# Kernel tuning notes

Hardware: AMD Instinct MI355X
Metric: run time of the kernel (lower is better)

Reference implementation:

```python
import jax, jax.numpy as jnp
import numpy as np

B, L, E = 64, 512, 512       # batch, encoder length, encoder dim
T = 512                      # decoder steps
S, P = 512, 256              # symbols_embedding_dim, prenet_dim
A, D = 1024, 1024            # attention_rnn_dim, decoder_rnn_dim
G, V = 128, 148              # gmm hidden, n_symbols


def setup_inputs() -> dict:
    key = jax.random.key(0)
    ks = jax.random.split(key, 20)
    w = lambda k, shp, s=0.02: (jax.random.normal(k, shp, dtype=jnp.float32) * s)
    memory = jax.random.normal(ks[0], (B, L, E), dtype=jnp.float32)
    decoder_inputs = jax.random.normal(ks[1], (B, S, T), dtype=jnp.float32)
    memory_lengths = jax.random.randint(ks[2], (B,), L // 2, L + 1)
    memory_lengths = memory_lengths.at[0].set(L)  # max length == L (static shapes)
    return {
        'memory': memory,
        'decoder_inputs': decoder_inputs,
        'memory_lengths': memory_lengths,
        'W_pre1': w(ks[3], (S, P)), 'W_pre2': w(ks[4], (P, P)),
        'W_att_ih': w(ks[5], (P + E, 4 * A)), 'W_att_hh': w(ks[6], (A, 4 * A)),
        'b_att_ih': jnp.zeros((4 * A,), jnp.float32), 'b_att_hh': jnp.zeros((4 * A,), jnp.float32),
        'W_g1': w(ks[7], (A, G)), 'b_g1': jnp.zeros((G,), jnp.float32),
        'W_g2': w(ks[8], (G, 2), 0.01),  # original inits this to zero; small random to exercise math
        'W_dec_ih': w(ks[9], (A + E, 4 * D)), 'W_dec_hh': w(ks[10], (D, 4 * D)),
        'b_dec_ih': jnp.zeros((4 * D,), jnp.float32), 'b_dec_hh': jnp.zeros((4 * D,), jnp.float32),
        'W_proj': w(ks[11], (D + E, V)), 'b_proj': jnp.zeros((V,), jnp.float32),
    }


def _lstm_cell(x, h, c, Wih, Whh, bih, bhh):
    # torch.nn.LSTMCell gate order: i, f, g, o
    g = x @ Wih + h @ Whh + bih + bhh
    i, f, gg, o = jnp.split(g, 4, axis=-1)
    c = jax.nn.sigmoid(f) * c + jax.nn.sigmoid(i) * jnp.tanh(gg)
    h = jax.nn.sigmoid(o) * jnp.tanh(c)
    return h, c


def _forward(memory, decoder_inputs, memory_lengths,
             W_pre1, W_pre2, W_att_ih, W_att_hh, b_att_ih, b_att_hh,
             W_g1, b_g1, W_g2, W_dec_ih, W_dec_hh, b_dec_ih, b_dec_hh,
             W_proj, b_proj):
    Bv, Sv, Tv = decoder_inputs.shape
    Lv = memory.shape[1]
    # go frame + teacher-forced inputs: (T+1, B, S)
    x = jnp.concatenate([jnp.zeros((1, Bv, Sv), memory.dtype),
                         jnp.transpose(decoder_inputs, (2, 0, 1))], axis=0)
    # Prenet: dropout is hardcoded training=True in the original
    dk1, dk2 = jax.random.split(jax.random.key(42))
    h1 = jax.nn.relu(x @ W_pre1)
    h1 = h1 * jax.random.bernoulli(dk1, 0.5, h1.shape).astype(h1.dtype) * 2.0
    h2 = jax.nn.relu(h1 @ W_pre2)
    pre = h2 * jax.random.bernoulli(dk2, 0.5, h2.shape).astype(h2.dtype) * 2.0  # (T+1,B,P)

    pad_mask = jnp.arange(Lv)[None, :] >= memory_lengths[:, None]  # (B,L) True on padding
    lin = jnp.arange(Lv, dtype=memory.dtype)[None, :]              # (1,L)

    Av, Dv, Ev = W_att_hh.shape[0], W_dec_hh.shape[0], memory.shape[2]
    init = (jnp.zeros((Bv, Av), memory.dtype), jnp.zeros((Bv, Av), memory.dtype),
            jnp.zeros((Bv, Dv), memory.dtype), jnp.zeros((Bv, Dv), memory.dtype),
            jnp.zeros((Bv, Lv), memory.dtype),  # cumulative attention weights
            jnp.zeros((Bv, Ev), memory.dtype),  # attention context
            jnp.zeros((Bv, 1), memory.dtype))   # GMM mean mu

    def step(carry, x_t):
        ah, ac, dh, dc, cum, ctx, mean = carry
        ah, ac = _lstm_cell(jnp.concatenate([x_t, ctx], -1), ah, ac,
                            W_att_ih, W_att_hh, b_att_ih, b_att_hh)
        # (eval mode: p_attention_dropout inactive)
        h = jnp.tanh(ah @ W_g1 + b_g1) @ W_g2          # (B,2) raw [mean_delta, scale]
        mean = mean + jnp.exp(h[:, :1]) * 8.0
        scale = jnp.exp(h[:, 1:]) * 8.0
        Z = jnp.sqrt(2.0 * np.pi * scale * scale)
        alpha = jnp.exp(-0.5 * (lin - mean) ** 2 / (scale * scale)) / Z  # (B,L)
        alpha = jnp.where(pad_mask, 0.0, alpha)
        ctx = jnp.einsum('bl,ble->be', alpha, memory)
        cum = cum + alpha
        dh, dc = _lstm_cell(jnp.concatenate([ah, ctx], -1), dh, dc,
                            W_dec_ih, W_dec_hh, b_dec_ih, b_dec_hh)
        logit = jnp.concatenate([dh, ctx], -1) @ W_proj + b_proj
        return (ah, ac, dh, dc, cum, ctx, mean), (logit, alpha, h)

    _, (logits, aligns, params) = jax.lax.scan(step, init, pre[:-1])
    return (jnp.transpose(logits, (1, 0, 2)),   # (B,T,V)
            jnp.transpose(aligns, (1, 0, 2)),   # (B,T,L)
            jnp.transpose(params, (1, 0, 2)))   # (B,T,2)


def reference(memory, decoder_inputs, memory_lengths, W_pre1, W_pre2,
              W_att_ih, W_att_hh, b_att_ih, b_att_hh, W_g1, b_g1, W_g2,
              W_dec_ih, W_dec_hh, b_dec_ih, b_dec_hh, W_proj, b_proj):
    return _forward(memory, decoder_inputs, memory_lengths, W_pre1, W_pre2,
                    W_att_ih, W_att_hh, b_att_ih, b_att_hh, W_g1, b_g1, W_g2,
                    W_dec_ih, W_dec_hh, b_dec_ih, b_dec_hh, W_proj, b_proj)
```

## Files before the change

### kernel.cpp

```cpp
#include <hip/hip_runtime.h>
#include <math.h>

#define TF_PARTITIONABLE 1

static constexpr int Bn=64, Ln=512, En=512, Tn=512, Sn=512, Pn=256, An=1024, Dn=1024, Gn=128, Vn=148;
static constexpr int G4A = 4096;
static constexpr int KPROJ = Dn + En;
static constexpr int KATT = 1792, KDEC = 2560;
static constexpr int ACH = 4, ACK = 448;
static constexpr int DCH = 4, DCK = 640;
static constexpr int NKB_ATT = KATT / 32;
static constexpr int NKB_DEC = KDEC / 32;
static constexpr long LOGITS_OFF = 0;
static constexpr long ALIGNS_OFF = (long)Bn*Tn*Vn;
static constexpr long PARAMS_OFF = ALIGNS_OFF + (long)Bn*Tn*Ln;

using s16x8 = __attribute__((ext_vector_type(8))) short;
using f32x4 = __attribute__((ext_vector_type(4))) float;

struct TFo { unsigned a, b; };
static constexpr TFo htf(unsigned k1, unsigned k2, unsigned x0, unsigned x1) {
  unsigned ks2 = k1 ^ k2 ^ 0x1BD11BDAu;
  unsigned ks[3] = {k1, k2, ks2};
  const unsigned ra[4] = {13u,15u,26u,6u}, rb[4] = {17u,29u,16u,24u};
  x0 += k1; x1 += k2;
  for (int g = 0; g < 5; ++g) {
    const unsigned* r = (g % 2 == 0) ? ra : rb;
    for (int i = 0; i < 4; ++i) { x0 += x1; x1 = (x1 << r[i]) | (x1 >> (32u - r[i])); x1 ^= x0; }
    x0 += ks[(g+1)%3]; x1 += ks[(g+2)%3] + (unsigned)(g+1);
  }
  return TFo{x0, x1};
}
#if TF_PARTITIONABLE
static constexpr TFo DK1 = htf(0u,42u,0u,0u);
static constexpr TFo DK2 = htf(0u,42u,0u,1u);
#else
static constexpr TFo S02 = htf(0u,42u,0u,2u);
static constexpr TFo S13 = htf(0u,42u,1u,3u);
static constexpr TFo DK1 = TFo{S02.a, S13.a};
static constexpr TFo DK2 = TFo{S02.b, S13.b};
#endif

__device__ __forceinline__ void dtf(unsigned k1, unsigned k2, unsigned x0, unsigned x1,
                                    unsigned& o0, unsigned& o1) {
  unsigned ks2 = k1 ^ k2 ^ 0x1BD11BDAu;
#define TFR(r) { x0 += x1; x1 = (x1<<r)|(x1>>(32-r)); x1 ^= x0; }
  x0 += k1; x1 += k2;
  TFR(13) TFR(15) TFR(26) TFR(6)  x0 += k2;  x1 += ks2 + 1u;
  TFR(17) TFR(29) TFR(16) TFR(24) x0 += ks2; x1 += k1 + 2u;
  TFR(13) TFR(15) TFR(26) TFR(6)  x0 += k1;  x1 += k2 + 3u;
  TFR(17) TFR(29) TFR(16) TFR(24) x0 += k2;  x1 += ks2 + 4u;
  TFR(13) TFR(15) TFR(26) TFR(6)  x0 += ks2; x1 += k1 + 5u;
#undef TFR
  o0 = x0; o1 = x1;
}

__device__ __forceinline__ bool keepmask(unsigned ka, unsigned kb, unsigned j) {
#if TF_PARTITIONABLE
  unsigned o0, o1; dtf(ka, kb, 0u, j, o0, o1);
  return ((o0 ^ o1) >> 31) == 0u;
#else
  const unsigned H = 4202496u;
  unsigned o0, o1;
  if (j < H) { dtf(ka, kb, j, j + H, o0, o1); return (o0 >> 31) == 0u; }
  else       { dtf(ka, kb, j - H, j, o0, o1); return (o1 >> 31) == 0u; }
#endif
}

__device__ __forceinline__ float ldbf(const unsigned short* p, long i) {
  return __uint_as_float(((unsigned)p[i]) << 16);
}
__device__ __forceinline__ unsigned short f2bf(float v) {
  unsigned x = __float_as_uint(v);
  return (unsigned short)((x + 0x7fffu + ((x >> 16) & 1u)) >> 16);
}
__device__ __forceinline__ void store_out(void* out, long i, float v, int bf) {
  if (bf) ((unsigned short*)out)[i] = f2bf(v);
  else    ((float*)out)[i] = v;
}
__device__ __forceinline__ float st_load(const float* p, long i) { return p[i]; }
__device__ __forceinline__ float st_load(const unsigned short* p, long i) { return ldbf(p, i); }
__device__ __forceinline__ void st_store(float* p, long i, float v) { p[i] = v; }
__device__ __forceinline__ void st_store(unsigned short* p, long i, float v) { p[i] = f2bf(v); }
__device__ __forceinline__ float sigm(float x) { return 1.f / (1.f + expf(-x)); }
__device__ __forceinline__ void st4bf(unsigned short* p, float a, float b, float c, float d) {
  union { unsigned short u[4]; uint2 v; } q;
  q.u[0] = f2bf(a); q.u[1] = f2bf(b); q.u[2] = f2bf(c); q.u[3] = f2bf(d);
  *(uint2*)p = q.v;
}
__device__ __forceinline__ void st8bf(unsigned short* p, const float* h) {
  union { unsigned short u[8]; uint4 v; } q;
#pragma unroll
  for (int i = 0; i < 8; ++i) q.u[i] = f2bf(h[i]);
  *(uint4*)p = q.v;
}

struct Ptrs {
  const float *Wp1,*Wp2,*bai,*bah,*Wg1,*bg1,*Wg2,*bdi,*bdh,*Wpr,*bpr;
  unsigned short *PWatt,*PWdec,*pre_bf,*attA,*decA;
  float *Patt,*Pdec,*ac,*dc,*mean;
  void *dh_all,*ctx_all;
  const void *mem,*din,*w_ai,*w_ah,*w_di,*w_dh;
  const int *mlen; const int *flag; void *out;
};

__global__ __launch_bounds__(256) void k_detect(const void* mem, int* flag) {
  __shared__ int cnt;
  int tid = threadIdx.x;
  if (tid == 0) cnt = 0;
  __syncthreads();
  const unsigned short* p = (const unsigned short*)mem;
  int local = 0;
  for (int i = tid; i < 1024; i += 256) {
    float f = ldbf(p, 2L * i);
    if (f == f && fabsf(f) > 0.0009f && fabsf(f) < 16.f) local++;
  }
  atomicAdd(&cnt, local);
  __syncthreads();
  if (tid == 0) flag[0] = (cnt > 512) ? 1 : 0;
}

__global__ __launch_bounds__(256) void k_convert(const void* src, float* dst, long n, const int* flag) {
  int bf = *flag;
  long i0 = (long)blockIdx.x * 256 + threadIdx.x, stp = (long)gridDim.x * 256;
  if (bf) { const unsigned short* s = (const unsigned short*)src;
            for (long i = i0; i < n; i += stp) dst[i] = ldbf(s, i); }
  else    { const float* s = (const float*)src;
            for (long i = i0; i < n; i += stp) dst[i] = s[i]; }
}

__global__ __launch_bounds__(256) void k_zero_f32(float* p, long n) {
  for (long i = (long)blockIdx.x * 256 + threadIdx.x; i < n; i += (long)gridDim.x * 256) p[i] = 0.f;
}

__global__ __launch_bounds__(256) void k_zero_aligns(void* out, const int* flag) {
  int bf = *flag;
  unsigned* p; long n;
  if (bf) { p = (unsigned*)out + (ALIGNS_OFF >> 1); n = ((long)Bn*Tn*Ln) >> 1; }
  else    { p = (unsigned*)out + ALIGNS_OFF;        n = (long)Bn*Tn*Ln; }
  for (long i = (long)blockIdx.x * 256 + threadIdx.x; i < n; i += (long)gridDim.x * 256) p[i] = 0u;
}

__global__ __launch_bounds__(256) void k_precopy(Ptrs P) {
  int tid = threadIdx.x;
  for (int i = tid; i < 2048; i += 256) {
    int b = i >> 5, g = i & 31;
    *(uint4*)(P.attA + (long)b * KATT + g * 8) =
        *(const uint4*)(P.pre_bf + (long)b * Pn + g * 8);
  }
}

__global__ __launch_bounds__(256) void k_pack(Ptrs P) {
  __shared__ float s[32][65];
  int bid = blockIdx.x, tid = threadIdx.x;
  bool att = bid < NKB_ATT * 64;
  int lb = att ? bid : bid - NKB_ATT * 64;
  int kblk = lb >> 6, ng = lb & 63;
  int n0 = ng * 64;
  int bf = *P.flag;
  int split = att ? (Pn + En) : (An + En);
  const void* S0 = att ? P.w_ai : P.w_di;
  const void* S1 = att ? P.w_ah : P.w_dh;
  for (int i = tid; i < 2048; i += 256) {
    int kk = i >> 6, n = i & 63;
    int k = kblk * 32 + kk;
    const void* src = (k < split) ? S0 : S1;
    long idx = (long)(k < split ? k : k - split) * G4A + (n0 + n);
    s[kk][n] = bf ? ldbf((const unsigned short*)src, idx) : ((const float*)src)[idx];
  }
  __syncthreads();
  int lane = tid & 63, tb = tid >> 6;
  unsigned short r[8];
#pragma unroll
  for (int j = 0; j < 8; ++j)
    r[j] = f2bf(s[(lane >> 4) * 8 + j][tb * 16 + (lane & 15)]);
  unsigned short* out = (att ? P.PWatt : P.PWdec) +
      (((long)kblk * 256 + (ng * 4 + tb)) * 64 + lane) * 8;
  *(uint4*)out = *(const uint4*)r;
}

__global__ __launch_bounds__(256) void k_prenet(Ptrs P, unsigned k1a, unsigned k1b,
                                                unsigned k2a, unsigned k2b) {
  __shared__ __align__(16) float x_s[32 * 17];
  __shared__ __align__(16) float W_s[16 * 256];
  __shared__ __align__(16) float h1_s[32 * 258];
  int bid = blockIdx.x, tid = threadIdx.x;
  int t = bid >> 1, half = bid & 1;
  int bf = *P.flag;
  int tc = tid & 63, tr = tid >> 6;
  int p0 = tc * 4, bl0 = tr * 8;
  float acc[8][4];
#pragma unroll
  for (int i = 0; i < 8; ++i) { acc[i][0]=0; acc[i][1]=0; acc[i][2]=0; acc[i][3]=0; }

  for (int kc = 0; kc < 32; ++kc) {
    __syncthreads();
    for (int i = tid; i < 32 * 16; i += 256) {
      int bl = i >> 4, kk = i & 15;
      int s = kc * 16 + kk;
      float v = 0.f;
      if (t > 0) {
        long idx = ((long)(half * 32 + bl) * Sn + s) * Tn + (t - 1);
        v = bf ? ldbf((const unsigned short*)P.din, idx) : ((const float*)P.din)[idx];
      }
      x_s[bl * 17 + kk] = v;
    }
    for (int i = tid; i < 16 * 256; i += 256) {
      int kk = i >> 8, p = i & 255;
      W_s[kk * 256 + p] = P.Wp1[(long)(kc * 16 + kk) * 256 + p];
    }
    __syncthreads();
    for (int kk = 0; kk < 16; ++kk) {
      float4 w = *(const float4*)(W_s + kk * 256 + p0);
#pragma unroll
      for (int i = 0; i < 8; ++i) {
        float x = x_s[(bl0 + i) * 17 + kk];
        acc[i][0] += x * w.x; acc[i][1] += x * w.y; acc[i][2] += x * w.z; acc[i][3] += x * w.w;
      }
    }
  }
#pragma unroll
  for (int i = 0; i < 8; ++i)
#pragma unroll
    for (int j = 0; j < 4; ++j) {
      int bl = bl0 + i, p = p0 + j, bg = half * 32 + bl;
      float v = fmaxf(acc[i][j], 0.f);
      unsigned ft = (unsigned)(((long)t * 64 + bg) * 256 + p);
      v = keepmask(k1a, k1b, ft) ? 2.f * v : 0.f;
      h1_s[bl * 258 + p] = v;
      acc[i][j] = 0.f;
    }
  __syncthreads();
  for (int kc = 0; kc < 16; ++kc) {
    __syncthreads();
    for (int i = tid; i < 16 * 256; i += 256) {
      int kk = i >> 8, p = i & 255;
      W_s[kk * 256 + p] = P.Wp2[(long)(kc * 16 + kk) * 256 + p];
    }
    __syncthreads();
    for (int kk = 0; kk < 16; ++kk) {
      float4 w = *(const float4*)(W_s + kk * 256 + p0);
      int s = kc * 16 + kk;
#pragma unroll
      for (int i = 0; i < 8; ++i) {
        float x = h1_s[(bl0 + i) * 258 + s];
        acc[i][0] += x * w.x; acc[i][1] += x * w.y; acc[i][2] += x * w.z; acc[i][3] += x * w.w;
      }
    }
  }
#pragma unroll
  for (int i = 0; i < 8; ++i)
#pragma unroll
    for (int j = 0; j < 4; ++j) {
      int bg = half * 32 + bl0 + i, p = p0 + j;
      float v = fmaxf(acc[i][j], 0.f);
      unsigned ft = (unsigned)(((long)t * 64 + bg) * 256 + p);
      v = keepmask(k2a, k2b, ft) ? 2.f * v : 0.f;
      P.pre_bf[((long)t * 64 + bg) * 256 + p] = f2bf(v);
    }
}

template<bool ATT>
__device__ __forceinline__ void dev_gemm(const Ptrs& P, int cg, int kc, unsigned short* a_lds) {
  constexpr int CK    = ATT ? ACK : DCK;
  constexpr int SUBK  = CK / 2;
  constexpr int NKS   = SUBK / 32;
  constexpr int PITCH = SUBK + 8;
  constexpr int GPR   = SUBK / 8;
  constexpr int KSTR  = ATT ? KATT : KDEC;
  int tid = threadIdx.x;
  int lane = tid & 63, w = tid >> 6;
  int nblk = cg * 4 + w;
  const unsigned short* PW = ATT ? P.PWatt : P.PWdec;
  const unsigned short* A  = ATT ? P.attA : P.decA;
  int rlo = lane & 15, khi8 = (lane >> 4) * 8;
  const int k0 = kc * CK;

  f32x4 acc[4];
#pragma unroll
  for (int i = 0; i < 4; ++i) acc[i] = f32x4{0.f, 0.f, 0.f, 0.f};

#pragma unroll
  for (int sub = 0; sub < 2; ++sub) {
    const int kk0 = k0 + sub * SUBK;
    __syncthreads();
#pragma unroll
    for (int i = 0; i < GPR / 4; ++i) {
      int g = tid + i * 256;
      int row = g / GPR, kg = (g - row * GPR) * 8;
      *(uint4*)(a_lds + row * PITCH + kg) = *(const uint4*)(A + (long)row * KSTR + kk0 + kg);
    }
    __syncthreads();
    const unsigned short* bptr = PW + (((long)(kk0 >> 5) * 256 + nblk) * 64 + lane) * 8;
    s16x8 br[4];
#pragma unroll
    for (int i = 0; i < 4; ++i) br[i] = *(const s16x8*)(bptr + (long)i * 131072);
#pragma unroll
    for (int kb = 0; kb < NKS; ++kb) {
      s16x8 bcur = br[kb & 3];
      if (kb + 4 < NKS) br[kb & 3] = *(const s16x8*)(bptr + (long)(kb + 4) * 131072);
      int abase = kb * 32 + khi8;
#pragma unroll
      for (int mb = 0; mb < 4; ++mb) {
        s16x8 a = *(const s16x8*)(a_lds + (mb * 16 + rlo) * PITCH + abase);
        acc[mb] = __builtin_amdgcn_mfma_f32_16x16x32_bf16(a, bcur, acc[mb], 0, 0, 0);
      }
    }
  }
  float* Pout = (ATT ? P.Patt : P.Pdec) + (long)kc * 64 * G4A;
  int col = nblk * 16 + rlo, rbase = (lane >> 4) * 4;
#pragma unroll
  for (int mb = 0; mb < 4; ++mb)
#pragma unroll
    for (int r = 0; r < 4; ++r)
      Pout[(long)(mb * 16 + rbase + r) * G4A + col] = acc[mb][r];
}

__global__ __launch_bounds__(256) void k_gemm(Ptrs P, int t) {
  __shared__ __align__(16) unsigned short a_lds[64 * 328];
  int bid = blockIdx.x;
  int low = bid & 7;
  int kc = low >> 1, p = low & 1;
  int rest = bid >> 3;
  bool att = rest < 32;
  int cg = (att ? rest : rest - 32) * 2 + p;
  if (att) { if (t + 1 < Tn) dev_gemm<true>(P, cg, kc, a_lds); }
  else     { if (t >= 0 && t < Tn) dev_gemm<false>(P, cg, kc, a_lds); }
}

template<typename ST>
__global__ __launch_bounds__(256) void k_point(Ptrs P, int t) {
  __shared__ float ah_s[1024];
  __shared__ float red_s[256];
  __shared__ float tanh_s[128];
  __shared__ float bc_s[2];
  __shared__ float alpha_s[176];
  int bid = blockIdx.x, tid = threadIdx.x;
  if (bid < 64) {
    if (t >= Tn) return;
    int b = bid;
    int bf = *P.flag;
    if (t + 1 < Tn && tid < 32) {
      *(uint4*)(P.attA + (long)b * KATT + tid * 8) =
          *(const uint4*)(P.pre_bf + ((long)(t + 1) * 64 + b) * Pn + tid * 8);
    }
    int u0 = tid * 4;
    float gv[4][4];
#pragma unroll
    for (int gt = 0; gt < 4; ++gt) {
      float4 a = *(const float4*)(P.bai + gt * 1024 + u0);
      float4 c = *(const float4*)(P.bah + gt * 1024 + u0);
      gv[gt][0] = a.x + c.x; gv[gt][1] = a.y + c.y; gv[gt][2] = a.z + c.z; gv[gt][3] = a.w + c.w;
    }
#pragma unroll
    for (int kc = 0; kc < ACH; ++kc) {
      const float* pa = P.Patt + ((long)kc * 64 + b) * G4A + u0;
#pragma unroll
      for (int gt = 0; gt < 4; ++gt) {
        float4 v = *(const float4*)(pa + gt * 1024);
        gv[gt][0] += v.x; gv[gt][1] += v.y; gv[gt][2] += v.z; gv[gt][3] += v.w;
      }
    }
    float4 oc = *(const float4*)(P.ac + b * 1024 + u0);
    float oldc[4] = {oc.x, oc.y, oc.z, oc.w};
    float hh[4], cc[4];
#pragma unroll
    for (int i = 0; i < 4; ++i) {
      float ii = sigm(gv[0][i]), ff = sigm(gv[1][i]), oo = sigm(gv[3][i]);
      cc[i] = ff * oldc[i] + ii * tanhf(gv[2][i]);
      hh[i] = oo * tanhf(cc[i]);
      ah_s[u0 + i] = hh[i];
    }
    *(float4*)(P.ac + b * 1024 + u0) = make_float4(cc[0], cc[1], cc[2], cc[3]);
    st4bf(P.attA + (long)b * KATT + 768 + u0, hh[0], hh[1], hh[2], hh[3]);
    st4bf(P.decA + (long)b * KDEC + u0,       hh[0], hh[1], hh[2], hh[3]);
    __syncthreads();
    {
      int g = tid & 127, hf = tid >> 7;
      const float* wg = P.Wg1 + g;
      float a0 = 0.f, a1 = 0.f;
      int ub = hf * 512;
      for (int u = ub; u < ub + 512; u += 2) {
        a0 += ah_s[u]     * wg[(long)u * 128];
        a1 += ah_s[u + 1] * wg[(long)(u + 1) * 128];
      }
      red_s[tid] = a0 + a1;
    }
    __syncthreads();
    if (tid < 128) tanh_s[tid] = tanhf(red_s[tid] + red_s[tid + 128] + P.bg1[tid]);
    __syncthreads();
    if (tid < 64) {
      float tv0 = tanh_s[tid], tv1 = tanh_s[tid + 64];
      float h0 = tv0 * P.Wg2[2 * tid]     + tv1 * P.Wg2[2 * (tid + 64)];
      float h1 = tv0 * P.Wg2[2 * tid + 1] + tv1 * P.Wg2[2 * (tid + 64) + 1];
#pragma unroll
      for (int o = 32; o; o >>= 1) { h0 += __shfl_down(h0, o); h1 += __shfl_down(h1, o); }
      if (tid == 0) {
        float m  = P.mean[b] + expf(h0) * 8.f;
        float sc = expf(h1) * 8.f;
        P.mean[b] = m;
        long pidx = PARAMS_OFF + ((long)b * Tn + t) * 2;
        store_out(P.out, pidx, h0, bf);
        store_out(P.out, pidx + 1, h1, bf);
        bc_s[0] = m; bc_s[1] = sc;
      }
    }
    __syncthreads();
    float m = bc_s[0], sc = bc_s[1];
    int len = P.mlen[b];
    int ci = (int)floorf(fminf(m, 100000.f));
    int l0 = ci - 80; if (l0 < 0) l0 = 0;
    int l1 = ci + 81; if (l1 > len) l1 = len;
    float inv2 = 0.5f / (sc * sc);
    float invZ = 1.f / (2.50662827463100050242f * sc);
    for (int l = l0 + tid; l < l1; l += 256) {
      float d = (float)l - m;
      float al = expf(-d * d * inv2) * invZ;
      alpha_s[l - l0] = al;
      store_out(P.out, ALIGNS_OFF + ((long)b * Tn + t) * Ln + l, al, bf);
    }
    __syncthreads();
    int nl = l1 - l0;
    ST* ctx_all = (ST*)P.ctx_all;
    int e0 = tid * 2;
    float s0 = 0.f, s1 = 0.f;
    if (bf) {
      const unsigned short* mem = (const unsigned short*)P.mem + ((long)b * Ln + l0) * En + e0;
      for (int l = 0; l < nl; ++l) {
        float al = alpha_s[l];
        s0 += al * ldbf(mem, (long)l * En);
        s1 += al * ldbf(mem, (long)l * En + 1);
      }
    } else {
      const float* mem = (const float*)P.mem + ((long)b * Ln + l0) * En + e0;
      for (int l = 0; l < nl; ++l) {
        float al = alpha_s[l];
        s0 += al * mem[(long)l * En];
        s1 += al * mem[(long)l * En + 1];
      }
    }
    unsigned q = (unsigned)f2bf(s0) | ((unsigned)f2bf(s1) << 16);
    *(unsigned*)(P.attA + (long)b * KATT + 256 + e0) = q;
    *(unsigned*)(P.decA + (long)b * KDEC + 1024 + e0) = q;
    st_store(ctx_all, ((long)t * 64 + b) * En + e0, s0);
    st_store(ctx_all, ((long)t * 64 + b) * En + e0 + 1, s1);
  } else {
    if (t == 0) return;
    int bb = bid - 64;
    int b = bb * 2 + (tid >> 7);
    int u0 = (tid & 127) * 8;
    ST* dh_all = (ST*)P.dh_all;
    float gv[4][8];
#pragma unroll
    for (int gt = 0; gt < 4; ++gt) {
      float4 a0 = *(const float4*)(P.bdi + gt * 1024 + u0);
      float4 a1 = *(const float4*)(P.bdi + gt * 1024 + u0 + 4);
      float4 c0 = *(const float4*)(P.bdh + gt * 1024 + u0);
      float4 c1 = *(const float4*)(P.bdh + gt * 1024 + u0 + 4);
      gv[gt][0] = a0.x + c0.x; gv[gt][1] = a0.y + c0.y; gv[gt][2] = a0.z + c0.z; gv[gt][3] = a0.w + c0.w;
      gv[gt][4] = a1.x + c1.x; gv[gt][5] = a1.y + c1.y; gv[gt][6] = a1.z + c1.z; gv[gt][7] = a1.w + c1.w;
    }
#pragma unroll
    for (int kc = 0; kc < DCH; ++kc) {
      const float* pd = P.Pdec + ((long)kc * 64 + b) * G4A + u0;
#pragma unroll
      for (int gt = 0; gt < 4; ++gt) {
        float4 v0 = *(const float4*)(pd + gt * 1024);
        float4 v1 = *(const float4*)(pd + gt * 1024 + 4);
        gv[gt][0] += v0.x; gv[gt][1] += v0.y; gv[gt][2] += v0.z; gv[gt][3] += v0.w;
        gv[gt][4] += v1.x; gv[gt][5] += v1.y; gv[gt][6] += v1.z; gv[gt][7] += v1.w;
      }
    }
    float4 oc0 = *(const float4*)(P.dc + b * 1024 + u0);
    float4 oc1 = *(const float4*)(P.dc + b * 1024 + u0 + 4);
    float oldc[8] = {oc0.x, oc0.y, oc0.z, oc0.w, oc1.x, oc1.y, oc1.z, oc1.w};
    float hh[8], cc[8];
#pragma unroll
    for (int i = 0; i < 8; ++i) {
      float ii = sigm(gv[0][i]), ff = sigm(gv[1][i]), oo = sigm(gv[3][i]);
      cc[i] = ff * oldc[i] + ii * tanhf(gv[2][i]);
      hh[i] = oo * tanhf(cc[i]);
    }
    *(float4*)(P.dc + b * 1024 + u0)     = make_float4(cc[0], cc[1], cc[2], cc[3]);
    *(float4*)(P.dc + b * 1024 + u0 + 4) = make_float4(cc[4], cc[5], cc[6], cc[7]);
    st8bf(P.decA + (long)b * KDEC + 1536 + u0, hh);
#pragma unroll
    for (int i = 0; i < 8; ++i)
      st_store(dh_all, ((long)(t - 1) * 64 + b) * 1024 + u0 + i, hh[i]);
  }
}

template<typename ST>
__global__ __launch_bounds__(256) void k_proj(Ptrs P) {
  __shared__ __align__(16) float A_s[64][65];
  __shared__ __align__(16) float W_s[64 * 160];
  int t = blockIdx.x, tid = threadIdx.x;
  int bf = *P.flag;
  const ST* dh_all = (const ST*)P.dh_all;
  const ST* ctx_all = (const ST*)P.ctx_all;
  int tc = tid & 15, tr = tid >> 4;
  int c0 = tc * 10, b0 = tr * 4;
  float acc[4][10];
#pragma unroll
  for (int i = 0; i < 4; ++i)
#pragma unroll
    for (int j = 0; j < 10; ++j) acc[i][j] = 0.f;
  for (int k0 = 0; k0 < KPROJ; k0 += 64) {
    __syncthreads();
    for (int i = tid; i < 64 * 64; i += 256) {
      int b = i >> 6, kk = i & 63;
      int k = k0 + kk;
      float v = (k < Dn) ? st_load(dh_all, ((long)t * 64 + b) * Dn + k)
                         : st_load(ctx_all, ((long)t * 64 + b) * En + (k - Dn));
      A_s[b][kk] = v;
    }
    for (int i = tid; i < 64 * 160; i += 256) {
      int kk = i / 160, c = i - kk * 160;
      W_s[kk * 160 + c] = (c < Vn) ? P.Wpr[(long)(k0 + kk) * Vn + c] : 0.f;
    }
    __syncthreads();
    for (int kk = 0; kk < 64; ++kk) {
      float xs[4];
#pragma unroll
      for (int i = 0; i < 4; ++i) xs[i] = A_s[b0 + i][kk];
#pragma unroll
      for (int j = 0; j < 10; ++j) {
        float w = W_s[kk * 160 + c0 + j];
#pragma unroll
        for (int i = 0; i < 4; ++i) acc[i][j] += xs[i] * w;
      }
    }
  }
#pragma unroll
  for (int i = 0; i < 4; ++i)
#pragma unroll
    for (int j = 0; j < 10; ++j) {
      int c = c0 + j;
      if (c < Vn) {
        int b = b0 + i;
        store_out(P.out, LOGITS_OFF + ((long)b * Tn + t) * Vn + c, acc[i][j] + P.bpr[c], bf);
      }
    }
}

template<typename ST>
static void run_pipeline(const Ptrs& P, hipStream_t stream) {
  k_prenet<<<Tn * 2, 256, 0, stream>>>(P, DK1.a, DK1.b, DK2.a, DK2.b);
  k_precopy<<<1, 256, 0, stream>>>(P);
  k_gemm<<<512, 256, 0, stream>>>(P, -1);
  for (int t = 0; t <= Tn; ++t) {
    k_point<ST><<<96, 256, 0, stream>>>(P, t);
    if (t < Tn) k_gemm<<<512, 256, 0, stream>>>(P, t);
  }
  k_proj<ST><<<Tn, 256, 0, stream>>>(P);
}

extern "C" void kernel_launch(void* const* d_in, const int* in_sizes, int n_in,
                              void* d_out, int out_size, void* d_ws, size_t ws_size,
                              hipStream_t stream) {
  (void)in_sizes; (void)n_in; (void)out_size;
  char* base = (char*)d_ws;
  int* flag = (int*)base;
  size_t off = 256;
  auto allocf = [&](size_t n) -> float* {
    float* p = (float*)(base + off);
    off += ((n * 4 + 255) / 256) * 256;
    return p;
  };
  auto allocu = [&](size_t n) -> unsigned short* {
    unsigned short* p = (unsigned short*)(base + off);
    off += ((n * 2 + 255) / 256) * 256;
    return p;
  };
  float* Wp1 = allocf(131072);
  float* Wp2 = allocf(65536);
  float* bai = allocf(4096);
  float* bah = allocf(4096);
  float* Wg1 = allocf(131072);
  float* bg1 = allocf(128);
  float* Wg2 = allocf(256);
  float* bdi = allocf(4096);
  float* bdh = allocf(4096);
  float* Wpr = allocf(227328);
  float* bpr = allocf(148);
  unsigned short* PWatt = allocu((size_t)NKB_ATT * 256 * 512);
  unsigned short* PWdec = allocu((size_t)NKB_DEC * 256 * 512);
  unsigned short* pre_bf = allocu((size_t)Tn * 64 * Pn);
  float* Patt = allocf((size_t)ACH * 64 * G4A);
  float* Pdec = allocf((size_t)DCH * 64 * G4A);
  float* ac = allocf(65536);
  float* dc = allocf(65536);
  float* mean = allocf(64);
  unsigned short* attA = allocu((size_t)64 * KATT);
  unsigned short* decA = allocu((size_t)64 * KDEC);
  size_t fixed = off;
  size_t nDH = (size_t)Tn * 64 * Dn, nCX = (size_t)Tn * 64 * En;
  bool f32tier = (fixed + (nDH + nCX) * 4 <= ws_size);
  bool b16tier = (fixed + (nDH + nCX) * 2 <= ws_size);
  if (!f32tier && !b16tier) return;

  Ptrs P;
  P.Wp1=Wp1; P.Wp2=Wp2; P.bai=bai; P.bah=bah; P.Wg1=Wg1; P.bg1=bg1; P.Wg2=Wg2;
  P.bdi=bdi; P.bdh=bdh; P.Wpr=Wpr; P.bpr=bpr;
  P.PWatt=PWatt; P.PWdec=PWdec; P.pre_bf=pre_bf; P.attA=attA; P.decA=decA;
  P.Patt=Patt; P.Pdec=Pdec; P.ac=ac; P.dc=dc; P.mean=mean;
  size_t esz = f32tier ? 4 : 2;
  P.dh_all  = base + fixed;
  P.ctx_all = base + fixed + nDH * esz;
  P.mem = d_in[0]; P.din = d_in[1]; P.mlen = (const int*)d_in[2];
  P.w_ai = d_in[5]; P.w_ah = d_in[6]; P.w_di = d_in[12]; P.w_dh = d_in[13];
  P.flag = flag; P.out = d_out;

  k_detect<<<1, 256, 0, stream>>>(d_in[0], flag);

  struct CV { const void* s; float* d; long n; };
  const CV cv[11] = {
    {d_in[3], Wp1, 131072}, {d_in[4], Wp2, 65536},
    {d_in[7], bai, 4096}, {d_in[8], bah, 4096},
    {d_in[9], Wg1, 131072}, {d_in[10], bg1, 128}, {d_in[11], Wg2, 256},
    {d_in[14], bdi, 4096}, {d_in[15], bdh, 4096},
    {d_in[16], Wpr, 227328}, {d_in[17], bpr, 148},
  };
  for (int i = 0; i < 11; ++i) {
    long g = (cv[i].n + 255) / 256; if (g > 1024) g = 1024;
    k_convert<<<(int)g, 256, 0, stream>>>(cv[i].s, cv[i].d, cv[i].n, flag);
  }
  k_pack<<<(NKB_ATT + NKB_DEC) * 64, 256, 0, stream>>>(P);
  k_zero_f32<<<512, 256, 0, stream>>>(ac, 131136 + 57344 + 81920);
  k_zero_aligns<<<2048, 256, 0, stream>>>(d_out, flag);

  if (f32tier) run_pipeline<float>(P, stream);
  else         run_pipeline<unsigned short>(P, stream);
}
```

Baseline: 15.43 ms.

## Split gate GEMM K dimension into 8 chunks and vectorize context loads

Doubles the number of K-chunks for the attention and decoder LSTM gate GEMMs, from 4 to 8, so each launch runs 1024 blocks instead of 512. Each block now processes one K-slice in a single LDS stage instead of two sub-stages. The aim is more parallelism per timestep on the latency-bound recurrent GEMM, at the cost of twice as many partial-sum outputs for the pointwise kernel to reduce. The context accumulation also loads bf16 and fp32 pairs as single 32-bit or float2 vectors.

```diff
diff --git a/kernel.cpp b/kernel.cpp
--- a/kernel.cpp
+++ b/kernel.cpp
@@ -7,8 +7,8 @@
 static constexpr int G4A = 4096;
 static constexpr int KPROJ = Dn + En;
 static constexpr int KATT = 1792, KDEC = 2560;
-static constexpr int ACH = 4, ACK = 448;
-static constexpr int DCH = 4, DCK = 640;
+static constexpr int ACH = 8, ACK = 224;
+static constexpr int DCH = 8, DCK = 320;
 static constexpr int NKB_ATT = KATT / 32;
 static constexpr int NKB_DEC = KDEC / 32;
 static constexpr long LOGITS_OFF = 0;
@@ -70,6 +70,8 @@
 __device__ __forceinline__ float ldbf(const unsigned short* p, long i) {
   return __uint_as_float(((unsigned)p[i]) << 16);
 }
+__device__ __forceinline__ float bflo(unsigned q) { return __uint_as_float(q << 16); }
+__device__ __forceinline__ float bfhi(unsigned q) { return __uint_as_float(q & 0xffff0000u); }
 __device__ __forceinline__ unsigned short f2bf(float v) {
   unsigned x = __float_as_uint(v);
   return (unsigned short)((x + 0x7fffu + ((x >> 16) & 1u)) >> 16);
@@ -263,10 +265,9 @@
 template<bool ATT>
 __device__ __forceinline__ void dev_gemm(const Ptrs& P, int cg, int kc, unsigned short* a_lds) {
   constexpr int CK    = ATT ? ACK : DCK;
-  constexpr int SUBK  = CK / 2;
-  constexpr int NKS   = SUBK / 32;
-  constexpr int PITCH = SUBK + 8;
-  constexpr int GPR   = SUBK / 8;
+  constexpr int NKS   = CK / 32;
+  constexpr int PITCH = CK + 8;
+  constexpr int GPR   = CK / 8;
   constexpr int KSTR  = ATT ? KATT : KDEC;
   int tid = threadIdx.x;
   int lane = tid & 63, w = tid >> 6;
@@ -281,30 +282,25 @@
   for (int i = 0; i < 4; ++i) acc[i] = f32x4{0.f, 0.f, 0.f, 0.f};
 
 #pragma unroll
-  for (int sub = 0; sub < 2; ++sub) {
-    const int kk0 = k0 + sub * SUBK;
-    __syncthreads();
-#pragma unroll
-    for (int i = 0; i < GPR / 4; ++i) {
-      int g = tid + i * 256;
-      int row = g / GPR, kg = (g - row * GPR) * 8;
-      *(uint4*)(a_lds + row * PITCH + kg) = *(const uint4*)(A + (long)row * KSTR + kk0 + kg);
-    }
-    __syncthreads();
-    const unsigned short* bptr = PW + (((long)(kk0 >> 5) * 256 + nblk) * 64 + lane) * 8;
-    s16x8 br[4];
-#pragma unroll
-    for (int i = 0; i < 4; ++i) br[i] = *(const s16x8*)(bptr + (long)i * 131072);
-#pragma unroll
-    for (int kb = 0; kb < NKS; ++kb) {
-      s16x8 bcur = br[kb & 3];
-      if (kb + 4 < NKS) br[kb & 3] = *(const s16x8*)(bptr + (long)(kb + 4) * 131072);
-      int abase = kb * 32 + khi8;
-#pragma unroll
-      for (int mb = 0; mb < 4; ++mb) {
-        s16x8 a = *(const s16x8*)(a_lds + (mb * 16 + rlo) * PITCH + abase);
-        acc[mb] = __builtin_amdgcn_mfma_f32_16x16x32_bf16(a, bcur, acc[mb], 0, 0, 0);
-      }
+  for (int i = 0; i < GPR / 4; ++i) {
+    int g = tid + i * 256;
+    int row = g / GPR, kg = (g - row * GPR) * 8;
+    *(uint4*)(a_lds + row * PITCH + kg) = *(const uint4*)(A + (long)row * KSTR + k0 + kg);
+  }
+  __syncthreads();
+  const unsigned short* bptr = PW + (((long)(k0 >> 5) * 256 + nblk) * 64 + lane) * 8;
+  s16x8 br[4];
+#pragma unroll
+  for (int i = 0; i < 4; ++i) br[i] = *(const s16x8*)(bptr + (long)i * 131072);
+#pragma unroll
+  for (int kb = 0; kb < NKS; ++kb) {
+    s16x8 bcur = br[kb & 3];
+    if (kb + 4 < NKS) br[kb & 3] = *(const s16x8*)(bptr + (long)(kb + 4) * 131072);
+    int abase = kb * 32 + khi8;
+#pragma unroll
+    for (int mb = 0; mb < 4; ++mb) {
+      s16x8 a = *(const s16x8*)(a_lds + (mb * 16 + rlo) * PITCH + abase);
+      acc[mb] = __builtin_amdgcn_mfma_f32_16x16x32_bf16(a, bcur, acc[mb], 0, 0, 0);
     }
   }
   float* Pout = (ATT ? P.Patt : P.Pdec) + (long)kc * 64 * G4A;
@@ -319,11 +315,9 @@
 __global__ __launch_bounds__(256) void k_gemm(Ptrs P, int t) {
   __shared__ __align__(16) unsigned short a_lds[64 * 328];
   int bid = blockIdx.x;
-  int low = bid & 7;
-  int kc = low >> 1, p = low & 1;
-  int rest = bid >> 3;
-  bool att = rest < 32;
-  int cg = (att ? rest : rest - 32) * 2 + p;
+  int kc = bid & 7;
+  bool att = bid < 512;
+  int cg = (att ? bid : bid - 512) >> 3;
   if (att) { if (t + 1 < Tn) dev_gemm<true>(P, cg, kc, a_lds); }
   else     { if (t >= 0 && t < Tn) dev_gemm<false>(P, cg, kc, a_lds); }
 }
@@ -425,18 +419,21 @@
     int e0 = tid * 2;
     float s0 = 0.f, s1 = 0.f;
     if (bf) {
-      const unsigned short* mem = (const unsigned short*)P.mem + ((long)b * Ln + l0) * En + e0;
+      const unsigned* mem = (const unsigned*)((const unsigned short*)P.mem +
+                                              ((long)b * Ln + l0) * En + e0);
       for (int l = 0; l < nl; ++l) {
         float al = alpha_s[l];
-        s0 += al * ldbf(mem, (long)l * En);
-        s1 += al * ldbf(mem, (long)l * En + 1);
+        unsigned q = mem[(long)l * (En / 2)];
+        s0 += al * bflo(q);
+        s1 += al * bfhi(q);
       }
     } else {
       const float* mem = (const float*)P.mem + ((long)b * Ln + l0) * En + e0;
       for (int l = 0; l < nl; ++l) {
         float al = alpha_s[l];
-        s0 += al * mem[(long)l * En];
-        s1 += al * mem[(long)l * En + 1];
+        float2 v = *(const float2*)(mem + (long)l * En);
+        s0 += al * v.x;
+        s1 += al * v.y;
       }
     }
     unsigned q = (unsigned)f2bf(s0) | ((unsigned)f2bf(s1) << 16);
@@ -547,10 +544,10 @@
 static void run_pipeline(const Ptrs& P, hipStream_t stream) {
   k_prenet<<<Tn * 2, 256, 0, stream>>>(P, DK1.a, DK1.b, DK2.a, DK2.b);
   k_precopy<<<1, 256, 0, stream>>>(P);
-  k_gemm<<<512, 256, 0, stream>>>(P, -1);
+  k_gemm<<<1024, 256, 0, stream>>>(P, -1);
   for (int t = 0; t <= Tn; ++t) {
     k_point<ST><<<96, 256, 0, stream>>>(P, t);
-    if (t < Tn) k_gemm<<<512, 256, 0, stream>>>(P, t);
+    if (t < Tn) k_gemm<<<1024, 256, 0, stream>>>(P, t);
   }
   k_proj<ST><<<Tn, 256, 0, stream>>>(P);
 }
```

Result: slower. 16.71 ms (+8.3%).

## Restructure recurrent step into two phases overlapping decoder GEMM with attention pointwise

Applied to the files above, without the earlier changes.

The per-step schedule changes. Before, a pointwise kernel (attention LSTM plus decoder LSTM) ran first, then a GEMM kernel for both LSTMs. Now phase 1 runs the decoder GEMM for step t-1 alongside the attention pointwise and GMM work for step t. Phase 2 runs the attention GEMM for step t+1 alongside the decoder pointwise for step t-1. The decoder input buffer is double-buffered by step parity so the two overlapping stages do not collide, and the context loop now loads bf16 pairs as one 32-bit word. The aim is to keep the short serial pointwise work off the critical path by co-scheduling it with GEMM blocks, at the cost of extra workspace and a more intricate step dependency.

```diff
diff --git a/kernel.cpp b/kernel.cpp
--- a/kernel.cpp
+++ b/kernel.cpp
@@ -70,6 +70,8 @@
 __device__ __forceinline__ float ldbf(const unsigned short* p, long i) {
   return __uint_as_float(((unsigned)p[i]) << 16);
 }
+__device__ __forceinline__ float bflo(unsigned q) { return __uint_as_float(q << 16); }
+__device__ __forceinline__ float bfhi(unsigned q) { return __uint_as_float(q & 0xffff0000u); }
 __device__ __forceinline__ unsigned short f2bf(float v) {
   unsigned x = __float_as_uint(v);
   return (unsigned short)((x + 0x7fffu + ((x >> 16) & 1u)) >> 16);
@@ -261,7 +263,8 @@
 }
 
 template<bool ATT>
-__device__ __forceinline__ void dev_gemm(const Ptrs& P, int cg, int kc, unsigned short* a_lds) {
+__device__ __forceinline__ void dev_gemm(const Ptrs& P, int cg, int kc,
+                                         const unsigned short* A, unsigned short* a_lds) {
   constexpr int CK    = ATT ? ACK : DCK;
   constexpr int SUBK  = CK / 2;
   constexpr int NKS   = SUBK / 32;
@@ -272,7 +275,6 @@
   int lane = tid & 63, w = tid >> 6;
   int nblk = cg * 4 + w;
   const unsigned short* PW = ATT ? P.PWatt : P.PWdec;
-  const unsigned short* A  = ATT ? P.attA : P.decA;
   int rlo = lane & 15, khi8 = (lane >> 4) * 8;
   const int k0 = kc * CK;
 
@@ -316,177 +318,198 @@
       Pout[(long)(mb * 16 + rbase + r) * G4A + col] = acc[mb][r];
 }
 
-__global__ __launch_bounds__(256) void k_gemm(Ptrs P, int t) {
+template<typename ST>
+__device__ __forceinline__ void dev_attpw(const Ptrs& P, int t, int b,
+    float* ah_s, float* red_s, float* tanh_s, float* bc_s, float* alpha_s) {
+  int tid = threadIdx.x;
+  int bf = *P.flag;
+  unsigned short* decAs = P.decA + (long)(t & 1) * 64 * KDEC;
+  if (t + 1 < Tn && tid < 32) {
+    *(uint4*)(P.attA + (long)b * KATT + tid * 8) =
+        *(const uint4*)(P.pre_bf + ((long)(t + 1) * 64 + b) * Pn + tid * 8);
+  }
+  int u0 = tid * 4;
+  float gv[4][4];
+#pragma unroll
+  for (int gt = 0; gt < 4; ++gt) {
+    float4 a = *(const float4*)(P.bai + gt * 1024 + u0);
+    float4 c = *(const float4*)(P.bah + gt * 1024 + u0);
+    gv[gt][0] = a.x + c.x; gv[gt][1] = a.y + c.y; gv[gt][2] = a.z + c.z; gv[gt][3] = a.w + c.w;
+  }
+#pragma unroll
+  for (int kc = 0; kc < ACH; ++kc) {
+    const float* pa = P.Patt + ((long)kc * 64 + b) * G4A + u0;
+#pragma unroll
+    for (int gt = 0; gt < 4; ++gt) {
+      float4 v = *(const float4*)(pa + gt * 1024);
+      gv[gt][0] += v.x; gv[gt][1] += v.y; gv[gt][2] += v.z; gv[gt][3] += v.w;
+    }
+  }
+  float4 oc = *(const float4*)(P.ac + b * 1024 + u0);
+  float oldc[4] = {oc.x, oc.y, oc.z, oc.w};
+  float hh[4], cc[4];
+#pragma unroll
+  for (int i = 0; i < 4; ++i) {
+    float ii = sigm(gv[0][i]), ff = sigm(gv[1][i]), oo = sigm(gv[3][i]);
+    cc[i] = ff * oldc[i] + ii * tanhf(gv[2][i]);
+    hh[i] = oo * tanhf(cc[i]);
+    ah_s[u0 + i] = hh[i];
+  }
+  *(float4*)(P.ac + b * 1024 + u0) = make_float4(cc[0], cc[1], cc[2], cc[3]);
+  st4bf(P.attA + (long)b * KATT + 768 + u0, hh[0], hh[1], hh[2], hh[3]);
+  st4bf(decAs + (long)b * KDEC + u0,        hh[0], hh[1], hh[2], hh[3]);
+  __syncthreads();
+  {
+    int g = tid & 127, hf = tid >> 7;
+    const float* wg = P.Wg1 + g;
+    float a0 = 0.f, a1 = 0.f;
+    int ub = hf * 512;
+    for (int u = ub; u < ub + 512; u += 2) {
+      a0 += ah_s[u]     * wg[(long)u * 128];
+      a1 += ah_s[u + 1] * wg[(long)(u + 1) * 128];
+    }
+    red_s[tid] = a0 + a1;
+  }
+  __syncthreads();
+  if (tid < 128) tanh_s[tid] = tanhf(red_s[tid] + red_s[tid + 128] + P.bg1[tid]);
+  __syncthreads();
+  if (tid < 64) {
+    float tv0 = tanh_s[tid], tv1 = tanh_s[tid + 64];
+    float h0 = tv0 * P.Wg2[2 * tid]     + tv1 * P.Wg2[2 * (tid + 64)];
+    float h1 = tv0 * P.Wg2[2 * tid + 1] + tv1 * P.Wg2[2 * (tid + 64) + 1];
+#pragma unroll
+    for (int o = 32; o; o >>= 1) { h0 += __shfl_down(h0, o); h1 += __shfl_down(h1, o); }
+    if (tid == 0) {
+      float m  = P.mean[b] + expf(h0) * 8.f;
+      float sc = expf(h1) * 8.f;
+      P.mean[b] = m;
+      long pidx = PARAMS_OFF + ((long)b * Tn + t) * 2;
+      store_out(P.out, pidx, h0, bf);
+      store_out(P.out, pidx + 1, h1, bf);
+      bc_s[0] = m; bc_s[1] = sc;
+    }
+  }
+  __syncthreads();
+  float m = bc_s[0], sc = bc_s[1];
+  int len = P.mlen[b];
+  int ci = (int)floorf(fminf(m, 100000.f));
+  int l0 = ci - 80; if (l0 < 0) l0 = 0;
+  int l1 = ci + 81; if (l1 > len) l1 = len;
+  float inv2 = 0.5f / (sc * sc);
+  float invZ = 1.f / (2.50662827463100050242f * sc);
+  for (int l = l0 + tid; l < l1; l += 256) {
+    float d = (float)l - m;
+    float al = expf(-d * d * inv2) * invZ;
+    alpha_s[l - l0] = al;
+    store_out(P.out, ALIGNS_OFF + ((long)b * Tn + t) * Ln + l, al, bf);
+  }
+  __syncthreads();
+  int nl = l1 - l0;
+  ST* ctx_all = (ST*)P.ctx_all;
+  int e0 = tid * 2;
+  float s0 = 0.f, s1 = 0.f;
+  if (bf) {
+    const unsigned* mem = (const unsigned*)((const unsigned short*)P.mem +
+                                            ((long)b * Ln + l0) * En + e0);
+    for (int l = 0; l < nl; ++l) {
+      float al = alpha_s[l];
+      unsigned q = mem[(long)l * (En / 2)];
+      s0 += al * bflo(q);
+      s1 += al * bfhi(q);
+    }
+  } else {
+    const float* mem = (const float*)P.mem + ((long)b * Ln + l0) * En + e0;
+    for (int l = 0; l < nl; ++l) {
+      float al = alpha_s[l];
+      float2 v = *(const float2*)(mem + (long)l * En);
+      s0 += al * v.x;
+      s1 += al * v.y;
+    }
+  }
+  unsigned q = (unsigned)f2bf(s0) | ((unsigned)f2bf(s1) << 16);
+  *(unsigned*)(P.attA + (long)b * KATT + 256 + e0) = q;
+  *(unsigned*)(decAs + (long)b * KDEC + 1024 + e0) = q;
+  st_store(ctx_all, ((long)t * 64 + b) * En + e0, s0);
+  st_store(ctx_all, ((long)t * 64 + b) * En + e0 + 1, s1);
+}
+
+template<typename ST>
+__device__ __forceinline__ void dev_decpw(const Ptrs& P, int tau, int bb) {
+  int tid = threadIdx.x;
+  int b = bb * 2 + (tid >> 7);
+  int u0 = (tid & 127) * 8;
+  ST* dh_all = (ST*)P.dh_all;
+  unsigned short* decAs = P.decA + (long)((tau + 1) & 1) * 64 * KDEC;
+  float gv[4][8];
+#pragma unroll
+  for (int gt = 0; gt < 4; ++gt) {
+    float4 a0 = *(const float4*)(P.bdi + gt * 1024 + u0);
+    float4 a1 = *(const float4*)(P.bdi + gt * 1024 + u0 + 4);
+    float4 c0 = *(const float4*)(P.bdh + gt * 1024 + u0);
+    float4 c1 = *(const float4*)(P.bdh + gt * 1024 + u0 + 4);
+    gv[gt][0] = a0.x + c0.x; gv[gt][1] = a0.y + c0.y; gv[gt][2] = a0.z + c0.z; gv[gt][3] = a0.w + c0.w;
+    gv[gt][4] = a1.x + c1.x; gv[gt][5] = a1.y + c1.y; gv[gt][6] = a1.z + c1.z; gv[gt][7] = a1.w + c1.w;
+  }
+#pragma unroll
+  for (int kc = 0; kc < DCH; ++kc) {
+    const float* pd = P.Pdec + ((long)kc * 64 + b) * G4A + u0;
+#pragma unroll
+    for (int gt = 0; gt < 4; ++gt) {
+      float4 v0 = *(const float4*)(pd + gt * 1024);
+      float4 v1 = *(const float4*)(pd + gt * 1024 + 4);
+      gv[gt][0] += v0.x; gv[gt][1] += v0.y; gv[gt][2] += v0.z; gv[gt][3] += v0.w;
+      gv[gt][4] += v1.x; gv[gt][5] += v1.y; gv[gt][6] += v1.z; gv[gt][7] += v1.w;
+    }
+  }
+  float4 oc0 = *(const float4*)(P.dc + b * 1024 + u0);
+  float4 oc1 = *(const float4*)(P.dc + b * 1024 + u0 + 4);
+  float oldc[8] = {oc0.x, oc0.y, oc0.z, oc0.w, oc1.x, oc1.y, oc1.z, oc1.w};
+  float hh[8], cc[8];
+#pragma unroll
+  for (int i = 0; i < 8; ++i) {
+    float ii = sigm(gv[0][i]), ff = sigm(gv[1][i]), oo = sigm(gv[3][i]);
+    cc[i] = ff * oldc[i] + ii * tanhf(gv[2][i]);
+    hh[i] = oo * tanhf(cc[i]);
+  }
+  *(float4*)(P.dc + b * 1024 + u0)     = make_float4(cc[0], cc[1], cc[2], cc[3]);
+  *(float4*)(P.dc + b * 1024 + u0 + 4) = make_float4(cc[4], cc[5], cc[6], cc[7]);
+  st8bf(decAs + (long)b * KDEC + 1536 + u0, hh);
+#pragma unroll
+  for (int i = 0; i < 8; ++i)
+    st_store(dh_all, ((long)tau * 64 + b) * 1024 + u0 + i, hh[i]);
+}
+
+template<typename ST>
+__global__ __launch_bounds__(256) void k_phase1(Ptrs P, int t) {
   __shared__ __align__(16) unsigned short a_lds[64 * 328];
-  int bid = blockIdx.x;
-  int low = bid & 7;
-  int kc = low >> 1, p = low & 1;
-  int rest = bid >> 3;
-  bool att = rest < 32;
-  int cg = (att ? rest : rest - 32) * 2 + p;
-  if (att) { if (t + 1 < Tn) dev_gemm<true>(P, cg, kc, a_lds); }
-  else     { if (t >= 0 && t < Tn) dev_gemm<false>(P, cg, kc, a_lds); }
-}
-
-template<typename ST>
-__global__ __launch_bounds__(256) void k_point(Ptrs P, int t) {
   __shared__ float ah_s[1024];
   __shared__ float red_s[256];
   __shared__ float tanh_s[128];
   __shared__ float bc_s[2];
   __shared__ float alpha_s[176];
-  int bid = blockIdx.x, tid = threadIdx.x;
-  if (bid < 64) {
+  int bid = blockIdx.x;
+  if (bid < 256) {
+    int tau = t - 1;
+    if (tau < 0 || tau >= Tn) return;
+    const unsigned short* A = P.decA + (long)(tau & 1) * 64 * KDEC;
+    dev_gemm<false>(P, bid >> 2, bid & 3, A, a_lds);
+  } else {
     if (t >= Tn) return;
-    int b = bid;
-    int bf = *P.flag;
-    if (t + 1 < Tn && tid < 32) {
-      *(uint4*)(P.attA + (long)b * KATT + tid * 8) =
-          *(const uint4*)(P.pre_bf + ((long)(t + 1) * 64 + b) * Pn + tid * 8);
-    }
-    int u0 = tid * 4;
-    float gv[4][4];
-#pragma unroll
-    for (int gt = 0; gt < 4; ++gt) {
-      float4 a = *(const float4*)(P.bai + gt * 1024 + u0);
-      float4 c = *(const float4*)(P.bah + gt * 1024 + u0);
-      gv[gt][0] = a.x + c.x; gv[gt][1] = a.y + c.y; gv[gt][2] = a.z + c.z; gv[gt][3] = a.w + c.w;
-    }
-#pragma unroll
-    for (int kc = 0; kc < ACH; ++kc) {
-      const float* pa = P.Patt + ((long)kc * 64 + b) * G4A + u0;
-#pragma unroll
-      for (int gt = 0; gt < 4; ++gt) {
-        float4 v = *(const float4*)(pa + gt * 1024);
-        gv[gt][0] += v.x; gv[gt][1] += v.y; gv[gt][2] += v.z; gv[gt][3] += v.w;
-      }
-    }
-    float4 oc = *(const float4*)(P.ac + b * 1024 + u0);
-    float oldc[4] = {oc.x, oc.y, oc.z, oc.w};
-    float hh[4], cc[4];
-#pragma unroll
-    for (int i = 0; i < 4; ++i) {
-      float ii = sigm(gv[0][i]), ff = sigm(gv[1][i]), oo = sigm(gv[3][i]);
-      cc[i] = ff * oldc[i] + ii * tanhf(gv[2][i]);
-      hh[i] = oo * tanhf(cc[i]);
-      ah_s[u0 + i] = hh[i];
-    }
-    *(float4*)(P.ac + b * 1024 + u0) = make_float4(cc[0], cc[1], cc[2], cc[3]);
-    st4bf(P.attA + (long)b * KATT + 768 + u0, hh[0], hh[1], hh[2], hh[3]);
-    st4bf(P.decA + (long)b * KDEC + u0,       hh[0], hh[1], hh[2], hh[3]);
-    __syncthreads();
-    {
-      int g = tid & 127, hf = tid >> 7;
-      const float* wg = P.Wg1 + g;
-      float a0 = 0.f, a1 = 0.f;
-      int ub = hf * 512;
-      for (int u = ub; u < ub + 512; u += 2) {
-        a0 += ah_s[u]     * wg[(long)u * 128];
-        a1 += ah_s[u + 1] * wg[(long)(u + 1) * 128];
-      }
-      red_s[tid] = a0 + a1;
-    }
-    __syncthreads();
-    if (tid < 128) tanh_s[tid] = tanhf(red_s[tid] + red_s[tid + 128] + P.bg1[tid]);
-    __syncthreads();
-    if (tid < 64) {
-      float tv0 = tanh_s[tid], tv1 = tanh_s[tid + 64];
-      float h0 = tv0 * P.Wg2[2 * tid]     + tv1 * P.Wg2[2 * (tid + 64)];
-      float h1 = tv0 * P.Wg2[2 * tid + 1] + tv1 * P.Wg2[2 * (tid + 64) + 1];
-#pragma unroll
-      for (int o = 32; o; o >>= 1) { h0 += __shfl_down(h0, o); h1 += __shfl_down(h1, o); }
-      if (tid == 0) {
-        float m  = P.mean[b] + expf(h0) * 8.f;
-        float sc = expf(h1) * 8.f;
-        P.mean[b] = m;
-        long pidx = PARAMS_OFF + ((long)b * Tn + t) * 2;
-        store_out(P.out, pidx, h0, bf);
-        store_out(P.out, pidx + 1, h1, bf);
-        bc_s[0] = m; bc_s[1] = sc;
-      }
-    }
-    __syncthreads();
-    float m = bc_s[0], sc = bc_s[1];
-    int len = P.mlen[b];
-    int ci = (int)floorf(fminf(m, 100000.f));
-    int l0 = ci - 80; if (l0 < 0) l0 = 0;
-    int l1 = ci + 81; if (l1 > len) l1 = len;
-    float inv2 = 0.5f / (sc * sc);
-    float invZ = 1.f / (2.50662827463100050242f * sc);
-    for (int l = l0 + tid; l < l1; l += 256) {
-      float d = (float)l - m;
-      float al = expf(-d * d * inv2) * invZ;
-      alpha_s[l - l0] = al;
-      store_out(P.out, ALIGNS_OFF + ((long)b * Tn + t) * Ln + l, al, bf);
-    }
-    __syncthreads();
-    int nl = l1 - l0;
-    ST* ctx_all = (ST*)P.ctx_all;
-    int e0 = tid * 2;
-    float s0 = 0.f, s1 = 0.f;
-    if (bf) {
-      const unsigned short* mem = (const unsigned short*)P.mem + ((long)b * Ln + l0) * En + e0;
-      for (int l = 0; l < nl; ++l) {
-        float al = alpha_s[l];
-        s0 += al * ldbf(mem, (long)l * En);
-        s1 += al * ldbf(mem, (long)l * En + 1);
-      }
-    } else {
-      const float* mem = (const float*)P.mem + ((long)b * Ln + l0) * En + e0;
-      for (int l = 0; l < nl; ++l) {
-        float al = alpha_s[l];
-        s0 += al * mem[(long)l * En];
-        s1 += al * mem[(long)l * En + 1];
-      }
-    }
-    unsigned q = (unsigned)f2bf(s0) | ((unsigned)f2bf(s1) << 16);
-    *(unsigned*)(P.attA + (long)b * KATT + 256 + e0) = q;
-    *(unsigned*)(P.decA + (long)b * KDEC + 1024 + e0) = q;
-    st_store(ctx_all, ((long)t * 64 + b) * En + e0, s0);
-    st_store(ctx_all, ((long)t * 64 + b) * En + e0 + 1, s1);
+    dev_attpw<ST>(P, t, bid - 256, ah_s, red_s, tanh_s, bc_s, alpha_s);
+  }
+}
+
+template<typename ST>
+__global__ __launch_bounds__(256) void k_phase2(Ptrs P, int t) {
+  __shared__ __align__(16) unsigned short a_lds[64 * 232];
+  int bid = blockIdx.x;
+  if (bid < 256) {
+    if (t + 1 < 0 || t + 1 >= Tn) return;
+    dev_gemm<true>(P, bid >> 2, bid & 3, P.attA, a_lds);
   } else {
-    if (t == 0) return;
-    int bb = bid - 64;
-    int b = bb * 2 + (tid >> 7);
-    int u0 = (tid & 127) * 8;
-    ST* dh_all = (ST*)P.dh_all;
-    float gv[4][8];
-#pragma unroll
-    for (int gt = 0; gt < 4; ++gt) {
-      float4 a0 = *(const float4*)(P.bdi + gt * 1024 + u0);
-      float4 a1 = *(const float4*)(P.bdi + gt * 1024 + u0 + 4);
-      float4 c0 = *(const float4*)(P.bdh + gt * 1024 + u0);
-      float4 c1 = *(const float4*)(P.bdh + gt * 1024 + u0 + 4);
-      gv[gt][0] = a0.x + c0.x; gv[gt][1] = a0.y + c0.y; gv[gt][2] = a0.z + c0.z; gv[gt][3] = a0.w + c0.w;
-      gv[gt][4] = a1.x + c1.x; gv[gt][5] = a1.y + c1.y; gv[gt][6] = a1.z + c1.z; gv[gt][7] = a1.w + c1.w;
-    }
-#pragma unroll
-    for (int kc = 0; kc < DCH; ++kc) {
-      const float* pd = P.Pdec + ((long)kc * 64 + b) * G4A + u0;
-#pragma unroll
-      for (int gt = 0; gt < 4; ++gt) {
-        float4 v0 = *(const float4*)(pd + gt * 1024);
-        float4 v1 = *(const float4*)(pd + gt * 1024 + 4);
-        gv[gt][0] += v0.x; gv[gt][1] += v0.y; gv[gt][2] += v0.z; gv[gt][3] += v0.w;
-        gv[gt][4] += v1.x; gv[gt][5] += v1.y; gv[gt][6] += v1.z; gv[gt][7] += v1.w;
-      }
-    }
-    float4 oc0 = *(const float4*)(P.dc + b * 1024 + u0);
-    float4 oc1 = *(const float4*)(P.dc + b * 1024 + u0 + 4);
-    float oldc[8] = {oc0.x, oc0.y, oc0.z, oc0.w, oc1.x, oc1.y, oc1.z, oc1.w};
-    float hh[8], cc[8];
-#pragma unroll
-    for (int i = 0; i < 8; ++i) {
-      float ii = sigm(gv[0][i]), ff = sigm(gv[1][i]), oo = sigm(gv[3][i]);
-      cc[i] = ff * oldc[i] + ii * tanhf(gv[2][i]);
-      hh[i] = oo * tanhf(cc[i]);
-    }
-    *(float4*)(P.dc + b * 1024 + u0)     = make_float4(cc[0], cc[1], cc[2], cc[3]);
-    *(float4*)(P.dc + b * 1024 + u0 + 4) = make_float4(cc[4], cc[5], cc[6], cc[7]);
-    st8bf(P.decA + (long)b * KDEC + 1536 + u0, hh);
-#pragma unroll
-    for (int i = 0; i < 8; ++i)
-      st_store(dh_all, ((long)(t - 1) * 64 + b) * 1024 + u0 + i, hh[i]);
+    int tau = t - 1;
+    if (tau < 0 || tau >= Tn) return;
+    dev_decpw<ST>(P, tau, bid - 256);
   }
 }
 
@@ -547,10 +570,10 @@
 static void run_pipeline(const Ptrs& P, hipStream_t stream) {
   k_prenet<<<Tn * 2, 256, 0, stream>>>(P, DK1.a, DK1.b, DK2.a, DK2.b);
   k_precopy<<<1, 256, 0, stream>>>(P);
-  k_gemm<<<512, 256, 0, stream>>>(P, -1);
+  k_phase2<ST><<<288, 256, 0, stream>>>(P, -1);
   for (int t = 0; t <= Tn; ++t) {
-    k_point<ST><<<96, 256, 0, stream>>>(P, t);
-    if (t < Tn) k_gemm<<<512, 256, 0, stream>>>(P, t);
+    k_phase1<ST><<<320, 256, 0, stream>>>(P, t);
+    k_phase2<ST><<<288, 256, 0, stream>>>(P, t);
   }
   k_proj<ST><<<Tn, 256, 0, stream>>>(P);
 }
@@ -592,7 +615,7 @@
   float* dc = allocf(65536);
   float* mean = allocf(64);
   unsigned short* attA = allocu((size_t)64 * KATT);
-  unsigned short* decA = allocu((size_t)64 * KDEC);
+  unsigned short* decA = allocu((size_t)2 * 64 * KDEC);
   size_t fixed = off;
   size_t nDH = (size_t)Tn * 64 * Dn, nCX = (size_t)Tn * 64 * En;
   bool f32tier = (fixed + (nDH + nCX) * 4 <= ws_size);
@@ -626,7 +649,7 @@
     k_convert<<<(int)g, 256, 0, stream>>>(cv[i].s, cv[i].d, cv[i].n, flag);
   }
   k_pack<<<(NKB_ATT + NKB_DEC) * 64, 256, 0, stream>>>(P);
-  k_zero_f32<<<512, 256, 0, stream>>>(ac, 131136 + 57344 + 81920);
+  k_zero_f32<<<512, 256, 0, stream>>>(ac, 131136 + 57344 + 163840);
   k_zero_aligns<<<2048, 256, 0, stream>>>(d_out, flag);
 
   if (f32tier) run_pipeline<float>(P, stream);
```

Result: slower. 15.76 ms (+2.1%).
